# Kernel optimization log

Measured on AMD Instinct MI355X. Metric: run time of the kernel, lower is better.

## Reference

```python
import jax, jax.numpy as jnp
import numpy as np

B, N, T, H = 16, 512, 100, 64

def setup_inputs() -> dict:
    key = jax.random.key(0)
    ks = jax.random.split(key, 9)
    s = 0.1
    return {
        "x": jax.random.normal(ks[0], (B, N, T), dtype=jnp.float32),
        "conv1_w": jax.random.normal(ks[1], (16, 1, 3), dtype=jnp.float32) * s,
        "conv1_b": jax.random.normal(ks[2], (16,), dtype=jnp.float32) * s,
        "conv2_w": jax.random.normal(ks[3], (32, 16, 3), dtype=jnp.float32) * s,
        "conv2_b": jax.random.normal(ks[4], (32,), dtype=jnp.float32) * s,
        "W_ih": jax.random.normal(ks[5], (3 * H, 32), dtype=jnp.float32) * s,
        "W_hh": jax.random.normal(ks[6], (3 * H, H), dtype=jnp.float32) * s,
        "b_ih": jax.random.normal(ks[7], (3 * H,), dtype=jnp.float32) * s,
        "b_hh": jax.random.normal(ks[8], (3 * H,), dtype=jnp.float32) * s,
    }

def _causal_conv_relu(h, w, b):
    # h: [BN, C_in, T]; left-pad (k-1)*dilation = 2 for causality
    y = jax.lax.conv_general_dilated(
        h, w, window_strides=(1,), padding=[(2, 0)],
        dimension_numbers=("NCH", "OIH", "NCH"))
    return jax.nn.relu(y + b[None, :, None])

def reference(x, conv1_w, conv1_b, conv2_w, conv2_b, W_ih, W_hh, b_ih, b_hh):
    b_, n_, t_ = x.shape
    h = x.reshape(b_ * n_, 1, t_)
    h = _causal_conv_relu(h, conv1_w, conv1_b)   # [BN, 16, T]
    h = _causal_conv_relu(h, conv2_w, conv2_b)   # [BN, 32, T]
    seq = h.transpose(0, 2, 1)                   # [BN, T, 32]
    # precompute input-to-gate projections for all timesteps: [BN, T, 3H]
    xp = jnp.einsum("btc,gc->btg", seq, W_ih) + b_ih
    hdim = W_hh.shape[1]

    def step(hprev, xt):
        gh = hprev @ W_hh.T + b_hh               # [BN, 3H]
        xr, xz, xn = jnp.split(xt, 3, axis=-1)
        hr, hz, hn = jnp.split(gh, 3, axis=-1)
        r = jax.nn.sigmoid(xr + hr)
        z = jax.nn.sigmoid(xz + hz)
        nn_ = jnp.tanh(xn + r * hn)
        hnew = (1.0 - z) * nn_ + z * hprev
        return hnew, None

    h0 = jnp.zeros((b_ * n_, hdim), dtype=x.dtype)
    hf, _ = jax.lax.scan(step, h0, xp.transpose(1, 0, 2))  # scan over T
    return hf.reshape(b_, n_, hdim)
```

## Files before the change

### kernel.cpp

```cpp
#include <hip/hip_runtime.h>
#include <stdint.h>

typedef __attribute__((ext_vector_type(8))) short s16x8;
typedef __attribute__((ext_vector_type(4))) float f32x4;

__device__ __forceinline__ short f2bf(float f){
  union { float f; uint32_t u; } v; v.f = f;
  uint32_t u = v.u;
  u += 0x7fffu + ((u >> 16) & 1u);
  return (short)(u >> 16);
}
__device__ __forceinline__ float sigm_fast(float x){
  float e = __builtin_amdgcn_exp2f(x * -1.44269504f);
  return __builtin_amdgcn_rcpf(1.f + e);
}
__device__ __forceinline__ float tanh_fast(float x){
  float e = __builtin_amdgcn_exp2f(x * 2.88539008f);
  return __builtin_fmaf(-2.f, __builtin_amdgcn_rcpf(e + 1.f), 1.f);
}

#define MFMA16(a, b, c) __builtin_amdgcn_mfma_f32_16x16x32_bf16((a), (b), (c), 0, 0, 0)

__global__ __launch_bounds__(256, 2) void te_fused(
    const float* __restrict__ x,
    const float* __restrict__ w1, const float* __restrict__ b1,
    const float* __restrict__ w2, const float* __restrict__ b2,
    const float* __restrict__ Wih, const float* __restrict__ Whh,
    const float* __restrict__ bih, const float* __restrict__ bhh,
    float* __restrict__ out)
{
  __shared__ float x_s[16 * 100];
  __shared__ short hA[2][16 * 72];
  __shared__ short c1b[16 * 328];
  __shared__ short s_b[16 * 640];

  const int tid  = threadIdx.x;
  const int lane = tid & 63;
  const int wv   = tid >> 6;
  const int l15  = lane & 15;
  const int lg   = lane >> 4;
  const int seq0 = blockIdx.x * 16;

  {
    const float4* gx = reinterpret_cast<const float4*>(x + (size_t)seq0 * 100);
    float4* sx = reinterpret_cast<float4*>(x_s);
    for (int i = tid; i < 400; i += 256) sx[i] = gx[i];
  }
  {
    int* p = reinterpret_cast<int*>(&hA[0][0]);
    for (int i = tid; i < 576; i += 256) p[i] = 0;
  }

  s16x8 WhhHi[3][2], WihHi[3];
  f32x4 bias_r, bias_z, bias_xn, bias_hn;
#pragma unroll
  for (int g = 0; g < 3; ++g) {
    const int n = 64 * g + 16 * wv + l15;
#pragma unroll
    for (int ks = 0; ks < 2; ++ks) {
      const float* p = Whh + n * 64 + ks * 32 + lg * 8;
#pragma unroll
      for (int j = 0; j < 8; ++j) WhhHi[g][ks][j] = f2bf(p[j]);
    }
    const float* q = Wih + n * 32 + lg * 8;
#pragma unroll
    for (int j = 0; j < 8; ++j) WihHi[g][j] = f2bf(q[j]);
    float bi = bih[n], bh = bhh[n];
    if (g == 0) { float v = bi + bh; bias_r  = (f32x4){v, v, v, v}; }
    if (g == 1) { float v = bi + bh; bias_z  = (f32x4){v, v, v, v}; }
    if (g == 2) { bias_xn = (f32x4){bi, bi, bi, bi};
                  bias_hn = (f32x4){bh, bh, bh, bh}; }
  }

  s16x8 cW2[2];
  f32x4 b2v4;
  {
    const int ch = 16 * (wv & 1) + l15;
    float bv = b2[ch];
    b2v4 = (f32x4){bv, bv, bv, bv};
#pragma unroll
    for (int ks = 0; ks < 2; ++ks) {
      s16x8 h8;
#pragma unroll
      for (int j = 0; j < 8; ++j) {
        const int k = ks * 32 + lg * 8 + j;
        const int g = k >> 4, ii = k & 15;
        h8[j] = (g < 3) ? f2bf(w2[ch * 48 + ii * 3 + g]) : (short)0;
      }
      cW2[ks] = h8;
    }
  }

  const int sl  = tid >> 4;
  const int chc = tid & 15;
  const float w1v0 = w1[chc * 3 + 0], w1v1 = w1[chc * 3 + 1], w1v2 = w1[chc * 3 + 2];
  const float b1v = b1[chc];

  const short* sRd  = &s_b[0]   + l15 * 40 + lg * 8;
  const short* hRd  = &hA[0][0] + l15 * 72 + lg * 8;
  short*       hWr  = &hA[0][0] + (lg * 4) * 72 + 16 * wv + l15;
  const short* c1Rd = &c1b[0]   + l15 * 328 + lg * 8;
  short*       sWr  = &s_b[0]   + (lg * 4) * 40 + (wv & 1) * 16 + l15;
  short*       c1Wr = &c1b[0]   + sl * 328 + chc;
  const float* xRd  = &x_s[sl * 100];
  const int    ub   = (wv >> 1) * 8;

  __syncthreads();

  float hreg[4] = {0.f, 0.f, 0.f, 0.f};

#define GSTEP(TL) do {                                                        \
    const int rb_ = (TL) & 1, wb_ = rb_ ^ 1;                                  \
    s16x8 as_ = *reinterpret_cast<const s16x8*>(sRd + (TL) * 640);            \
    s16x8 ah0 = *reinterpret_cast<const s16x8*>(hRd + rb_ * 1152);            \
    s16x8 ah1 = *reinterpret_cast<const s16x8*>(hRd + rb_ * 1152 + 32);       \
    __builtin_amdgcn_s_setprio(1);                                            \
    f32x4 pr = MFMA16(as_, WihHi[0],                                          \
               MFMA16(ah1, WhhHi[0][1],                                       \
               MFMA16(ah0, WhhHi[0][0], bias_r)));                            \
    f32x4 pz = MFMA16(as_, WihHi[1],                                          \
               MFMA16(ah1, WhhHi[1][1],                                       \
               MFMA16(ah0, WhhHi[1][0], bias_z)));                            \
    f32x4 xn = MFMA16(as_, WihHi[2], bias_xn);                                \
    f32x4 hn = MFMA16(ah1, WhhHi[2][1],                                       \
               MFMA16(ah0, WhhHi[2][0], bias_hn));                            \
    __builtin_amdgcn_s_setprio(0);                                            \
    float hnew[4];                                                            \
    _Pragma("unroll")                                                         \
    for (int i2 = 0; i2 < 4; ++i2) {                                          \
      float r = sigm_fast(pr[i2]);                                            \
      float z = sigm_fast(pz[i2]);                                            \
      float tn = tanh_fast(__builtin_fmaf(r, hn[i2], xn[i2]));                \
      float h = __builtin_fmaf(z, hreg[i2] - tn, tn);                         \
      hreg[i2] = h; hnew[i2] = h;                                             \
    }                                                                         \
    uint32_t p01, p23;                                                        \
    asm("v_cvt_pk_bf16_f32 %0, %1, %2" : "=v"(p01) : "v"(hnew[0]), "v"(hnew[1])); \
    asm("v_cvt_pk_bf16_f32 %0, %1, %2" : "=v"(p23) : "v"(hnew[2]), "v"(hnew[3])); \
    hWr[wb_ * 1152 +   0] = (short)(p01 & 0xffff);                            \
    hWr[wb_ * 1152 +  72] = (short)(p01 >> 16);                               \
    hWr[wb_ * 1152 + 144] = (short)(p23 & 0xffff);                            \
    hWr[wb_ * 1152 + 216] = (short)(p23 >> 16);                               \
    __syncthreads();                                                          \
  } while (0)

#pragma unroll 1
  for (int k = 0; k < 7; ++k) {
    const int t0 = k * 16;

    {
      int xi0 = t0 - 4, xi1 = t0 - 3;
      float xa = (xi0 < 0) ? 0.f : xRd[xi0 < 0 ? 0 : xi0];
      float xb = (xi1 < 0) ? 0.f : xRd[xi1 < 0 ? 0 : xi1];
#pragma unroll
      for (int i = 0; i < 19; ++i) {
        const int xi = t0 - 2 + i;
        const int idx = xi < 0 ? 0 : (xi > 99 ? 99 : xi);
        float xv = xRd[idx];
        float xc = (xi < 0) ? 0.f : xv;
        float c = __builtin_fmaf(w1v0, xa,
                  __builtin_fmaf(w1v1, xb,
                  __builtin_fmaf(w1v2, xc, b1v)));
        c = c > 0.f ? c : 0.f;
        c = (xi < 0) ? 0.f : c;
        uint32_t cu;
        asm("v_cvt_pk_bf16_f32 %0, %1, %2" : "=v"(cu) : "v"(c), "v"(c));
        c1Wr[i * 16] = (short)(cu & 0xffff);
        xa = xb; xb = xc;
      }
    }
    __syncthreads();

    {
#pragma unroll
      for (int i = 0; i < 8; ++i) {
        const int u = ub + i;
        s16x8 a0 = *reinterpret_cast<const s16x8*>(c1Rd + u * 16);
        s16x8 a1 = *reinterpret_cast<const s16x8*>(c1Rd + u * 16 + 32);
        f32x4 sa = MFMA16(a1, cW2[1], MFMA16(a0, cW2[0], b2v4));
        float m0 = sa[0] > 0.f ? sa[0] : 0.f;
        float m1 = sa[1] > 0.f ? sa[1] : 0.f;
        float m2 = sa[2] > 0.f ? sa[2] : 0.f;
        float m3 = sa[3] > 0.f ? sa[3] : 0.f;
        uint32_t u01, u23;
        asm("v_cvt_pk_bf16_f32 %0, %1, %2" : "=v"(u01) : "v"(m0), "v"(m1));
        asm("v_cvt_pk_bf16_f32 %0, %1, %2" : "=v"(u23) : "v"(m2), "v"(m3));
        sWr[u * 640 +   0] = (short)(u01 & 0xffff);
        sWr[u * 640 +  40] = (short)(u01 >> 16);
        sWr[u * 640 +  80] = (short)(u23 & 0xffff);
        sWr[u * 640 + 120] = (short)(u23 >> 16);
      }
    }
    __syncthreads();

    if (k < 6) {
      GSTEP(0);  GSTEP(1);  GSTEP(2);  GSTEP(3);
      GSTEP(4);  GSTEP(5);  GSTEP(6);  GSTEP(7);
      GSTEP(8);  GSTEP(9);  GSTEP(10); GSTEP(11);
      GSTEP(12); GSTEP(13); GSTEP(14); GSTEP(15);
    } else {
      GSTEP(0);  GSTEP(1);  GSTEP(2);  GSTEP(3);
    }
  }

#pragma unroll
  for (int i2 = 0; i2 < 4; ++i2) {
    out[(size_t)(seq0 + lg * 4 + i2) * 64 + 16 * wv + l15] = hreg[i2];
  }
}

extern "C" void kernel_launch(void* const* d_in, const int* in_sizes, int n_in,
                              void* d_out, int out_size, void* d_ws, size_t ws_size,
                              hipStream_t stream)
{
  (void)in_sizes; (void)n_in; (void)d_ws; (void)ws_size; (void)out_size;
  const float* x   = (const float*)d_in[0];
  const float* w1  = (const float*)d_in[1];
  const float* b1  = (const float*)d_in[2];
  const float* w2  = (const float*)d_in[3];
  const float* b2  = (const float*)d_in[4];
  const float* Wih = (const float*)d_in[5];
  const float* Whh = (const float*)d_in[6];
  const float* bih = (const float*)d_in[7];
  const float* bhh = (const float*)d_in[8];
  float* out = (float*)d_out;
  te_fused<<<512, 256, 0, stream>>>(x, w1, b1, w2, b2, Wih, Whh, bih, bhh, out);
}
```

Before: 74.64 us.

## Interleave two independent GRU sequence groups per block to hide recurrence latency

Each block now handles 32 sequences as two independent 16-sequence groups. The MFMA gate phase of one group is interleaved with the elementwise activation phase of the other, so the serial GRU dependency chain can overlap across groups. Conv stages are batched for both groups, the grid is halved, and launch bounds drop to one block per CU. The trade-off is fewer blocks (256 on a 256-CU-class device), more registers and LDS per block, and a more complex, skewed pipeline with a final epilogue step for group B.

```diff
diff --git a/kernel.cpp b/kernel.cpp
--- a/kernel.cpp
+++ b/kernel.cpp
@@ -21,7 +21,7 @@
 
 #define MFMA16(a, b, c) __builtin_amdgcn_mfma_f32_16x16x32_bf16((a), (b), (c), 0, 0, 0)
 
-__global__ __launch_bounds__(256, 2) void te_fused(
+__global__ __launch_bounds__(256, 1) void te_fused(
     const float* __restrict__ x,
     const float* __restrict__ w1, const float* __restrict__ b1,
     const float* __restrict__ w2, const float* __restrict__ b2,
@@ -29,26 +29,28 @@
     const float* __restrict__ bih, const float* __restrict__ bhh,
     float* __restrict__ out)
 {
-  __shared__ float x_s[16 * 100];
-  __shared__ short hA[2][16 * 72];
-  __shared__ short c1b[16 * 328];
-  __shared__ short s_b[16 * 640];
+  __shared__ float x_s[32 * 100];
+  __shared__ short hS[2][2][16 * 72];
+  __shared__ short c1b[2][16 * 328];
+  __shared__ short s_b[2][16 * 640];
 
   const int tid  = threadIdx.x;
   const int lane = tid & 63;
   const int wv   = tid >> 6;
   const int l15  = lane & 15;
   const int lg   = lane >> 4;
-  const int seq0 = blockIdx.x * 16;
+  const int seq0 = blockIdx.x * 32;
 
   {
     const float4* gx = reinterpret_cast<const float4*>(x + (size_t)seq0 * 100);
     float4* sx = reinterpret_cast<float4*>(x_s);
-    for (int i = tid; i < 400; i += 256) sx[i] = gx[i];
+    for (int i = tid; i < 800; i += 256) sx[i] = gx[i];
   }
   {
-    int* p = reinterpret_cast<int*>(&hA[0][0]);
+    int* p = reinterpret_cast<int*>(&hS[0][0][0]);
     for (int i = tid; i < 576; i += 256) p[i] = 0;
+    int* q = reinterpret_cast<int*>(&hS[1][0][0]);
+    for (int i = tid; i < 576; i += 256) q[i] = 0;
   }
 
   s16x8 WhhHi[3][2], WihHi[3];
@@ -72,10 +74,12 @@
                   bias_hn = (f32x4){bh, bh, bh, bh}; }
   }
 
+  const int cq  = wv >> 1;
+  const int cnt = wv & 1;
   s16x8 cW2[2];
   f32x4 b2v4;
   {
-    const int ch = 16 * (wv & 1) + l15;
+    const int ch = 16 * cnt + l15;
     float bv = b2[ch];
     b2v4 = (f32x4){bv, bv, bv, bv};
 #pragma unroll
@@ -96,116 +100,149 @@
   const float w1v0 = w1[chc * 3 + 0], w1v1 = w1[chc * 3 + 1], w1v2 = w1[chc * 3 + 2];
   const float b1v = b1[chc];
 
-  const short* sRd  = &s_b[0]   + l15 * 40 + lg * 8;
-  const short* hRd  = &hA[0][0] + l15 * 72 + lg * 8;
-  short*       hWr  = &hA[0][0] + (lg * 4) * 72 + 16 * wv + l15;
-  const short* c1Rd = &c1b[0]   + l15 * 328 + lg * 8;
-  short*       sWr  = &s_b[0]   + (lg * 4) * 40 + (wv & 1) * 16 + l15;
-  short*       c1Wr = &c1b[0]   + sl * 328 + chc;
-  const float* xRd  = &x_s[sl * 100];
-  const int    ub   = (wv >> 1) * 8;
+  const short* sRdA = &s_b[0][0] + l15 * 40 + lg * 8;
+  const short* sRdB = &s_b[1][0] + l15 * 40 + lg * 8;
+  const short* hRdA = &hS[0][0][0] + l15 * 72 + lg * 8;
+  const short* hRdB = &hS[1][0][0] + l15 * 72 + lg * 8;
+  short* hWrA = &hS[0][0][0] + (lg * 4) * 72 + 16 * wv + l15;
+  short* hWrB = &hS[1][0][0] + (lg * 4) * 72 + 16 * wv + l15;
+  const short* c1Rd = &c1b[cq][0] + l15 * 328 + lg * 8;
+  short* sWrC = &s_b[cq][0] + (lg * 4) * 40 + cnt * 16 + l15;
+  short* c1WrA = &c1b[0][0] + sl * 328 + chc;
+  short* c1WrB = &c1b[1][0] + sl * 328 + chc;
+  const float* xRdA = &x_s[sl * 100];
+  const float* xRdB = &x_s[(sl + 16) * 100];
 
   __syncthreads();
 
-  float hreg[4] = {0.f, 0.f, 0.f, 0.f};
-
-#define GSTEP(TL) do {                                                        \
-    const int rb_ = (TL) & 1, wb_ = rb_ ^ 1;                                  \
-    s16x8 as_ = *reinterpret_cast<const s16x8*>(sRd + (TL) * 640);            \
-    s16x8 ah0 = *reinterpret_cast<const s16x8*>(hRd + rb_ * 1152);            \
-    s16x8 ah1 = *reinterpret_cast<const s16x8*>(hRd + rb_ * 1152 + 32);       \
-    __builtin_amdgcn_s_setprio(1);                                            \
-    f32x4 pr = MFMA16(as_, WihHi[0],                                          \
-               MFMA16(ah1, WhhHi[0][1],                                       \
-               MFMA16(ah0, WhhHi[0][0], bias_r)));                            \
-    f32x4 pz = MFMA16(as_, WihHi[1],                                          \
-               MFMA16(ah1, WhhHi[1][1],                                       \
-               MFMA16(ah0, WhhHi[1][0], bias_z)));                            \
-    f32x4 xn = MFMA16(as_, WihHi[2], bias_xn);                                \
-    f32x4 hn = MFMA16(ah1, WhhHi[2][1],                                       \
-               MFMA16(ah0, WhhHi[2][0], bias_hn));                            \
-    __builtin_amdgcn_s_setprio(0);                                            \
+  float hregA[4] = {0.f, 0.f, 0.f, 0.f};
+  float hregB[4] = {0.f, 0.f, 0.f, 0.f};
+  f32x4 prA, pzA, xnA, hnA, prB, pzB, xnB, hnB;
+  int hOffA = 0, hOffB = 0;
+
+#define MPHASE(sPtr_, hBase_, hOff_, PR_, PZ_, XN_, HN_) do {                 \
+    s16x8 as_ = *reinterpret_cast<const s16x8*>(sPtr_);                       \
+    s16x8 ah0 = *reinterpret_cast<const s16x8*>((hBase_) + (hOff_));          \
+    s16x8 ah1 = *reinterpret_cast<const s16x8*>((hBase_) + (hOff_) + 32);     \
+    PR_ = MFMA16(as_, WihHi[0],                                               \
+          MFMA16(ah1, WhhHi[0][1],                                            \
+          MFMA16(ah0, WhhHi[0][0], bias_r)));                                 \
+    PZ_ = MFMA16(as_, WihHi[1],                                               \
+          MFMA16(ah1, WhhHi[1][1],                                            \
+          MFMA16(ah0, WhhHi[1][0], bias_z)));                                 \
+    XN_ = MFMA16(as_, WihHi[2], bias_xn);                                     \
+    HN_ = MFMA16(ah1, WhhHi[2][1],                                            \
+          MFMA16(ah0, WhhHi[2][0], bias_hn));                                 \
+  } while (0)
+
+#define EPHASE(PR_, PZ_, XN_, HN_, HREG_, hWr_, hOffW_) do {                  \
     float hnew[4];                                                            \
     _Pragma("unroll")                                                         \
     for (int i2 = 0; i2 < 4; ++i2) {                                          \
-      float r = sigm_fast(pr[i2]);                                            \
-      float z = sigm_fast(pz[i2]);                                            \
-      float tn = tanh_fast(__builtin_fmaf(r, hn[i2], xn[i2]));                \
-      float h = __builtin_fmaf(z, hreg[i2] - tn, tn);                         \
-      hreg[i2] = h; hnew[i2] = h;                                             \
+      float r = sigm_fast(PR_[i2]);                                           \
+      float z = sigm_fast(PZ_[i2]);                                           \
+      float tn = tanh_fast(__builtin_fmaf(r, HN_[i2], XN_[i2]));              \
+      float h = __builtin_fmaf(z, HREG_[i2] - tn, tn);                        \
+      HREG_[i2] = h; hnew[i2] = h;                                            \
     }                                                                         \
     uint32_t p01, p23;                                                        \
     asm("v_cvt_pk_bf16_f32 %0, %1, %2" : "=v"(p01) : "v"(hnew[0]), "v"(hnew[1])); \
     asm("v_cvt_pk_bf16_f32 %0, %1, %2" : "=v"(p23) : "v"(hnew[2]), "v"(hnew[3])); \
-    hWr[wb_ * 1152 +   0] = (short)(p01 & 0xffff);                            \
-    hWr[wb_ * 1152 +  72] = (short)(p01 >> 16);                               \
-    hWr[wb_ * 1152 + 144] = (short)(p23 & 0xffff);                            \
-    hWr[wb_ * 1152 + 216] = (short)(p23 >> 16);                               \
-    __syncthreads();                                                          \
+    (hWr_)[(hOffW_) +   0] = (short)(p01 & 0xffff);                           \
+    (hWr_)[(hOffW_) +  72] = (short)(p01 >> 16);                              \
+    (hWr_)[(hOffW_) + 144] = (short)(p23 & 0xffff);                           \
+    (hWr_)[(hOffW_) + 216] = (short)(p23 >> 16);                              \
   } while (0)
 
 #pragma unroll 1
   for (int k = 0; k < 7; ++k) {
     const int t0 = k * 16;
+    const int NS = (k < 6) ? 16 : 4;
 
     {
       int xi0 = t0 - 4, xi1 = t0 - 3;
-      float xa = (xi0 < 0) ? 0.f : xRd[xi0 < 0 ? 0 : xi0];
-      float xb = (xi1 < 0) ? 0.f : xRd[xi1 < 0 ? 0 : xi1];
+      float xaA = (xi0 < 0) ? 0.f : xRdA[xi0];
+      float xbA = (xi1 < 0) ? 0.f : xRdA[xi1];
+      float xaB = (xi0 < 0) ? 0.f : xRdB[xi0];
+      float xbB = (xi1 < 0) ? 0.f : xRdB[xi1];
 #pragma unroll
       for (int i = 0; i < 19; ++i) {
         const int xi = t0 - 2 + i;
         const int idx = xi < 0 ? 0 : (xi > 99 ? 99 : xi);
-        float xv = xRd[idx];
-        float xc = (xi < 0) ? 0.f : xv;
-        float c = __builtin_fmaf(w1v0, xa,
-                  __builtin_fmaf(w1v1, xb,
-                  __builtin_fmaf(w1v2, xc, b1v)));
-        c = c > 0.f ? c : 0.f;
-        c = (xi < 0) ? 0.f : c;
+        float xcA = (xi < 0) ? 0.f : xRdA[idx];
+        float xcB = (xi < 0) ? 0.f : xRdB[idx];
+        float cA = __builtin_fmaf(w1v0, xaA,
+                   __builtin_fmaf(w1v1, xbA,
+                   __builtin_fmaf(w1v2, xcA, b1v)));
+        cA = cA > 0.f ? cA : 0.f;
+        cA = (xi < 0) ? 0.f : cA;
+        float cB = __builtin_fmaf(w1v0, xaB,
+                   __builtin_fmaf(w1v1, xbB,
+                   __builtin_fmaf(w1v2, xcB, b1v)));
+        cB = cB > 0.f ? cB : 0.f;
+        cB = (xi < 0) ? 0.f : cB;
         uint32_t cu;
-        asm("v_cvt_pk_bf16_f32 %0, %1, %2" : "=v"(cu) : "v"(c), "v"(c));
-        c1Wr[i * 16] = (short)(cu & 0xffff);
-        xa = xb; xb = xc;
+        asm("v_cvt_pk_bf16_f32 %0, %1, %2" : "=v"(cu) : "v"(cA), "v"(cB));
+        c1WrA[i * 16] = (short)(cu & 0xffff);
+        c1WrB[i * 16] = (short)(cu >> 16);
+        xaA = xbA; xbA = xcA; xaB = xbB; xbB = xcB;
       }
     }
     __syncthreads();
 
-    {
-#pragma unroll
-      for (int i = 0; i < 8; ++i) {
-        const int u = ub + i;
-        s16x8 a0 = *reinterpret_cast<const s16x8*>(c1Rd + u * 16);
-        s16x8 a1 = *reinterpret_cast<const s16x8*>(c1Rd + u * 16 + 32);
-        f32x4 sa = MFMA16(a1, cW2[1], MFMA16(a0, cW2[0], b2v4));
-        float m0 = sa[0] > 0.f ? sa[0] : 0.f;
-        float m1 = sa[1] > 0.f ? sa[1] : 0.f;
-        float m2 = sa[2] > 0.f ? sa[2] : 0.f;
-        float m3 = sa[3] > 0.f ? sa[3] : 0.f;
-        uint32_t u01, u23;
-        asm("v_cvt_pk_bf16_f32 %0, %1, %2" : "=v"(u01) : "v"(m0), "v"(m1));
-        asm("v_cvt_pk_bf16_f32 %0, %1, %2" : "=v"(u23) : "v"(m2), "v"(m3));
-        sWr[u * 640 +   0] = (short)(u01 & 0xffff);
-        sWr[u * 640 +  40] = (short)(u01 >> 16);
-        sWr[u * 640 +  80] = (short)(u23 & 0xffff);
-        sWr[u * 640 + 120] = (short)(u23 >> 16);
-      }
-    }
-    __syncthreads();
-
-    if (k < 6) {
-      GSTEP(0);  GSTEP(1);  GSTEP(2);  GSTEP(3);
-      GSTEP(4);  GSTEP(5);  GSTEP(6);  GSTEP(7);
-      GSTEP(8);  GSTEP(9);  GSTEP(10); GSTEP(11);
-      GSTEP(12); GSTEP(13); GSTEP(14); GSTEP(15);
-    } else {
-      GSTEP(0);  GSTEP(1);  GSTEP(2);  GSTEP(3);
-    }
+#pragma unroll
+    for (int u = 0; u < 16; ++u) {
+      s16x8 a0 = *reinterpret_cast<const s16x8*>(c1Rd + u * 16);
+      s16x8 a1 = *reinterpret_cast<const s16x8*>(c1Rd + u * 16 + 32);
+      f32x4 sa = MFMA16(a1, cW2[1], MFMA16(a0, cW2[0], b2v4));
+      float m0 = sa[0] > 0.f ? sa[0] : 0.f;
+      float m1 = sa[1] > 0.f ? sa[1] : 0.f;
+      float m2 = sa[2] > 0.f ? sa[2] : 0.f;
+      float m3 = sa[3] > 0.f ? sa[3] : 0.f;
+      uint32_t u01, u23;
+      asm("v_cvt_pk_bf16_f32 %0, %1, %2" : "=v"(u01) : "v"(m0), "v"(m1));
+      asm("v_cvt_pk_bf16_f32 %0, %1, %2" : "=v"(u23) : "v"(m2), "v"(m3));
+      sWrC[u * 640 +   0] = (short)(u01 & 0xffff);
+      sWrC[u * 640 +  40] = (short)(u01 >> 16);
+      sWrC[u * 640 +  80] = (short)(u23 & 0xffff);
+      sWrC[u * 640 + 120] = (short)(u23 >> 16);
+    }
+    __syncthreads();
+
+    const short* sA = sRdA;
+    const short* sB = sRdB;
+
+    MPHASE(sA, hRdA, hOffA, prA, pzA, xnA, hnA); sA += 640;
+    if (k > 0) { EPHASE(prB, pzB, xnB, hnB, hregB, hWrB, hOffB ^ 1152); hOffB ^= 1152; }
+    __syncthreads();
+
+#pragma unroll 2
+    for (int j = 0; j < NS - 1; ++j) {
+      MPHASE(sB, hRdB, hOffB, prB, pzB, xnB, hnB); sB += 640;
+      EPHASE(prA, pzA, xnA, hnA, hregA, hWrA, hOffA ^ 1152); hOffA ^= 1152;
+      __syncthreads();
+      MPHASE(sA, hRdA, hOffA, prA, pzA, xnA, hnA); sA += 640;
+      EPHASE(prB, pzB, xnB, hnB, hregB, hWrB, hOffB ^ 1152); hOffB ^= 1152;
+      __syncthreads();
+    }
+
+    MPHASE(sB, hRdB, hOffB, prB, pzB, xnB, hnB);
+    EPHASE(prA, pzA, xnA, hnA, hregA, hWrA, hOffA ^ 1152); hOffA ^= 1152;
+    __syncthreads();
   }
 
 #pragma unroll
   for (int i2 = 0; i2 < 4; ++i2) {
-    out[(size_t)(seq0 + lg * 4 + i2) * 64 + 16 * wv + l15] = hreg[i2];
+    float r = sigm_fast(prB[i2]);
+    float z = sigm_fast(pzB[i2]);
+    float tn = tanh_fast(__builtin_fmaf(r, hnB[i2], xnB[i2]));
+    hregB[i2] = __builtin_fmaf(z, hregB[i2] - tn, tn);
+  }
+
+#pragma unroll
+  for (int i2 = 0; i2 < 4; ++i2) {
+    out[(size_t)(seq0 + lg * 4 + i2) * 64 + 16 * wv + l15] = hregA[i2];
+    out[(size_t)(seq0 + 16 + lg * 4 + i2) * 64 + 16 * wv + l15] = hregB[i2];
   }
 }
 
@@ -224,5 +261,5 @@
   const float* bih = (const float*)d_in[7];
   const float* bhh = (const float*)d_in[8];
   float* out = (float*)d_out;
-  te_fused<<<512, 256, 0, stream>>>(x, w1, b1, w2, b2, Wih, Whh, bih, bhh, out);
-}
+  te_fused<<<256, 256, 0, stream>>>(x, w1, b1, w2, b2, Wih, Whh, bih, bhh, out);
+}
```

Result: slower. 97.30 us (+30.4%).
